# Kernel optimization log

Hardware: AMD Instinct MI355X
Metric: run time of the kernel (lower is better)

Reference implementation:

```python
import jax, jax.numpy as jnp
import numpy as np

# module constants (match init_kwargs)
D_MODEL = 1024
N_HEADS = 16
D_K = 64
CHUNK_LEN = 64
EPS = 1e-8

B, C, N, NL = 4, 16, 2, 128  # batch, chunks, neighbors, neighbor_len
S = C * CHUNK_LEN            # seq_len = 1024


def setup_inputs() -> dict:
    key = jax.random.key(0)
    ks = jax.random.split(key, 10)
    s = 0.02
    HD = N_HEADS * D_K
    return {
        "h": jax.random.normal(ks[0], (B, S, D_MODEL), jnp.float32),
        "e": jax.random.normal(ks[1], (B, C, N, NL, D_MODEL), jnp.float32),
        "g_norm": jnp.ones((D_MODEL,), jnp.float32),
        "Wq": jax.random.normal(ks[2], (D_MODEL, HD), jnp.float32) * s,
        "bq": jnp.zeros((HD,), jnp.float32),
        "Wk": jax.random.normal(ks[3], (D_MODEL, HD), jnp.float32) * s,
        "bk": jnp.zeros((HD,), jnp.float32),
        "Wv": jax.random.normal(ks[4], (D_MODEL, HD), jnp.float32) * s,
        "bv": jnp.zeros((HD,), jnp.float32),
        "Wo": jax.random.normal(ks[5], (HD, D_MODEL), jnp.float32) * s,
        "bo": jnp.zeros((D_MODEL,), jnp.float32),
    }


def _rmsnorm(x, g):
    return x * g * jax.lax.rsqrt(jnp.mean(x * x, axis=-1, keepdims=True) + EPS)


def reference(h, e, g_norm, Wq, bq, Wk, bk, Wv, bv, Wo, bo):
    b, seq, d = h.shape
    _, c, n, nl, _ = e.shape
    cl = CHUNK_LEN
    scale = 1.0 / np.sqrt(D_K).astype(np.float32)

    h_res = h
    hn = _rmsnorm(h[:, cl - 1:], g_norm)                 # [b, seq-cl+1, d]
    pad = c * cl - hn.shape[1]
    hn = jnp.pad(hn, ((0, 0), (0, pad), (0, 0)))         # [b, c*cl, d]
    hn = hn.reshape(b, c, cl, d)

    q = (hn @ Wq + bq).reshape(b, c, cl, N_HEADS, D_K)       # bcihd
    k = (e @ Wk + bk).reshape(b, c, n, nl, N_HEADS, D_K)     # bcnjhd
    v = (e @ Wv + bv).reshape(b, c, n, nl, N_HEADS, D_K)

    attn = jnp.einsum('bcihd,bcnjhd->bchinj', q, k) * scale  # [b,c,h,i,n,j]
    attn = jax.nn.softmax(attn.reshape(b, c, N_HEADS, cl, n * nl), axis=-1)
    attn = attn.reshape(b, c, N_HEADS, cl, n, nl)

    o = jnp.einsum('bchinj,bcnjhd->bcihd', attn, v)
    o = o.reshape(b, c * cl, N_HEADS * D_K)
    o = o @ Wo + bo                                          # [b, c*cl, d]
    o = jnp.pad(o, ((0, 0), (cl - 1, 0), (0, 0)))            # shift right by cl-1
    return o[:, :seq] + h_res
```

## Files before the change

kernel.cpp:

```cpp
#include <hip/hip_runtime.h>
#include <stdint.h>

#define DEV __device__ __forceinline__

typedef __attribute__((ext_vector_type(8))) __bf16 bf16x8;
typedef __attribute__((ext_vector_type(4))) float floatx4;

DEV float bf2f(unsigned short u) {
  union { unsigned int i; float f; } x; x.i = ((unsigned int)u) << 16; return x.f;
}
DEV unsigned int f2bf(float f) {
  union { float f; unsigned int i; } x; x.f = f;
  unsigned int r = x.i + 0x7FFFu + ((x.i >> 16) & 1u);
  return r >> 16;
}
DEV void gl2lds16(const unsigned short* g, unsigned short* l) {
  __builtin_amdgcn_global_load_lds(
      (const __attribute__((address_space(1))) unsigned int*)g,
      (__attribute__((address_space(3))) unsigned int*)l, 16, 0, 0);
}
DEV floatx4 zero4() { floatx4 z; z[0]=0.f; z[1]=0.f; z[2]=0.f; z[3]=0.f; return z; }

__global__ void cca_f2b_k(const float* __restrict__ x,
                          unsigned short* __restrict__ y) {
  int i = blockIdx.x * 256 + threadIdx.x;
  float4 v = ((const float4*)x)[i];
  uint2 o;
  o.x = f2bf(v.x) | (f2bf(v.y) << 16);
  o.y = f2bf(v.z) | (f2bf(v.w) << 16);
  ((uint2*)y)[i] = o;
}

__global__ void cca_transpose_k(const float* __restrict__ W,
                                unsigned short* __restrict__ Wt, int K, int N) {
  __shared__ float tile[64][65];
  int k0 = blockIdx.x * 64, n0 = blockIdx.y * 64;
  int t = threadIdx.x;
  int c = t & 63, r4 = t >> 6;
#pragma unroll
  for (int it = 0; it < 16; ++it) {
    int r = it * 4 + r4;
    tile[r][c] = W[(size_t)(k0 + r) * N + n0 + c];
  }
  __syncthreads();
#pragma unroll
  for (int it = 0; it < 16; ++it) {
    int r = it * 4 + r4;
    Wt[(size_t)(n0 + r) * K + k0 + c] = (unsigned short)f2bf(tile[c][r]);
  }
}

__global__ void cca_rmsnorm_k(const float* __restrict__ h,
                              const float* __restrict__ g,
                              unsigned short* __restrict__ hn) {
  int row = blockIdx.x;
  int b = row >> 10, p = row & 1023;
  int t = threadIdx.x;
  unsigned short* dst = hn + (size_t)row * 1024;
  if (p >= 961) {
    uint2 z; z.x = 0u; z.y = 0u;
    ((uint2*)dst)[t] = z;
    return;
  }
  const float* src = h + ((size_t)(b << 10) + p + 63) * 1024;
  float4 v = ((const float4*)src)[t];
  float ss = v.x*v.x + v.y*v.y + v.z*v.z + v.w*v.w;
#pragma unroll
  for (int m = 32; m > 0; m >>= 1) ss += __shfl_down(ss, m);
  __shared__ float wsum[4];
  int lane = t & 63, wv = t >> 6;
  if (lane == 0) wsum[wv] = ss;
  __syncthreads();
  float tot = wsum[0] + wsum[1] + wsum[2] + wsum[3];
  float r = rsqrtf(tot * (1.0f / 1024.0f) + 1e-8f);
  float4 gv = ((const float4*)g)[t];
  uint2 outp;
  outp.x = f2bf(v.x * gv.x * r) | (f2bf(v.y * gv.y * r) << 16);
  outp.y = f2bf(v.z * gv.z * r) | (f2bf(v.w * gv.w * r) << 16);
  ((uint2*)dst)[t] = outp;
}

template <int MODE>
__launch_bounds__(256, 2)
__global__ void cca_gemm_k(const unsigned short* __restrict__ A,
                           const unsigned short* __restrict__ Bt,
                           const float* __restrict__ bias1,
                           const float* __restrict__ bias2,
                           const float* __restrict__ resid,
                           void* __restrict__ Cout,
                           int M, int N, int K) {
  __shared__ unsigned short Ash[128 * 32];
  __shared__ unsigned short Bsh[128 * 32];
  int tM = blockIdx.x * 128, tN = blockIdx.y * 128;
  int t = threadIdx.x, lane = t & 63, wv = t >> 6;
  int wm = wv >> 1, wn = wv & 1;
  int l15 = lane & 15, quad = lane >> 4;
  int arow = lane >> 2, achk = lane & 3;
  floatx4 acc[4][4];
#pragma unroll
  for (int i = 0; i < 4; ++i)
#pragma unroll
    for (int j = 0; j < 4; ++j) acc[i][j] = zero4();

  for (int k0 = 0; k0 < K; k0 += 32) {
    __syncthreads();
#pragma unroll
    for (int ii = 0; ii < 2; ++ii) {
      int seg = wv + ii * 4;
      int row = seg * 16 + arow;
      gl2lds16(A + (size_t)(tM + row) * K + k0 + achk * 8, Ash + seg * 512);
      gl2lds16(Bt + (size_t)(tN + row) * K + k0 + achk * 8, Bsh + seg * 512);
    }
    __syncthreads();
    bf16x8 af[4], bfv[4];
#pragma unroll
    for (int mt = 0; mt < 4; ++mt)
      af[mt] = *(const bf16x8*)&Ash[(wm * 64 + mt * 16 + l15) * 32 + quad * 8];
#pragma unroll
    for (int nt = 0; nt < 4; ++nt)
      bfv[nt] = *(const bf16x8*)&Bsh[(wn * 64 + nt * 16 + l15) * 32 + quad * 8];
#pragma unroll
    for (int mt = 0; mt < 4; ++mt)
#pragma unroll
      for (int nt = 0; nt < 4; ++nt)
        acc[mt][nt] = __builtin_amdgcn_mfma_f32_16x16x32_bf16(af[mt], bfv[nt], acc[mt][nt], 0, 0, 0);
  }

#pragma unroll
  for (int mt = 0; mt < 4; ++mt) {
    int mrow = tM + wm * 64 + mt * 16 + quad * 4;
#pragma unroll
    for (int nt = 0; nt < 4; ++nt) {
      int ncol = tN + wn * 64 + nt * 16 + l15;
      float bs;
      if (MODE == 0) {
        bs = (bias2 != nullptr && ncol >= 1024) ? bias2[ncol - 1024] : bias1[ncol];
      } else {
        bs = bias1[ncol];
      }
#pragma unroll
      for (int r = 0; r < 4; ++r) {
        int m = mrow + r;
        float v = acc[mt][nt][r] + bs;
        if (MODE == 0) {
          ((unsigned short*)Cout)[(size_t)m * N + ncol] = (unsigned short)f2bf(v);
        } else {
          int p = m & 1023;
          if (p < 961) {
            size_t o = (size_t)(m + 63) * 1024 + (size_t)ncol;
            ((float*)Cout)[o] = v + resid[o];
          }
        }
      }
    }
  }
}

__launch_bounds__(256, 1)
__global__ void cca_attn_k(const unsigned short* __restrict__ Q,
                           const unsigned short* __restrict__ KV,
                           unsigned short* __restrict__ O) {
  __shared__ unsigned short Qsh[64 * 64];
  __shared__ unsigned short Ksh[256 * 64];
  __shared__ unsigned short VT[64 * 264];
  __shared__ unsigned short Psh[64 * 264];
  int bch = blockIdx.x;
  int hh = bch & 15, c = (bch >> 4) & 15, b = bch >> 8;
  int t = threadIdx.x, lane = t & 63, wv = t >> 6;
  int l15 = lane & 15, quad = lane >> 4;
  size_t qbase = (size_t)b * 1024 + (size_t)c * 64;
  size_t kvbase = (size_t)b * 4096 + (size_t)c * 256;
  int hoff = hh * 64;

  {
    int rowi = lane >> 3, chk = lane & 7;
#pragma unroll
    for (int ii = 0; ii < 2; ++ii) {
      int seg = wv + ii * 4;
      int row = seg * 8 + rowi;
      gl2lds16(Q + (qbase + row) * 1024 + hoff + chk * 8, Qsh + seg * 512);
    }
#pragma unroll
    for (int ii = 0; ii < 8; ++ii) {
      int seg = wv + ii * 4;
      int row = seg * 8 + rowi;
      gl2lds16(KV + (kvbase + row) * 2048 + hoff + chk * 8, Ksh + seg * 512);
    }
  }
  {
    const unsigned short* vp = KV + (kvbase + t) * 2048 + 1024 + hoff;
#pragma unroll
    for (int d0 = 0; d0 < 64; d0 += 8) {
      uint4 raw = *(const uint4*)(vp + d0);
      unsigned int w0 = raw.x, w1 = raw.y, w2 = raw.z, w3 = raw.w;
      VT[(d0 + 0) * 264 + t] = (unsigned short)(w0 & 0xffff);
      VT[(d0 + 1) * 264 + t] = (unsigned short)(w0 >> 16);
      VT[(d0 + 2) * 264 + t] = (unsigned short)(w1 & 0xffff);
      VT[(d0 + 3) * 264 + t] = (unsigned short)(w1 >> 16);
      VT[(d0 + 4) * 264 + t] = (unsigned short)(w2 & 0xffff);
      VT[(d0 + 5) * 264 + t] = (unsigned short)(w2 >> 16);
      VT[(d0 + 6) * 264 + t] = (unsigned short)(w3 & 0xffff);
      VT[(d0 + 7) * 264 + t] = (unsigned short)(w3 >> 16);
    }
  }
  __syncthreads();

  floatx4 st[16];
#pragma unroll
  for (int i = 0; i < 16; ++i) st[i] = zero4();
  bf16x8 a0 = *(const bf16x8*)&Qsh[(wv * 16 + l15) * 64 + quad * 8];
  bf16x8 a1 = *(const bf16x8*)&Qsh[(wv * 16 + l15) * 64 + 32 + quad * 8];
#pragma unroll
  for (int kt = 0; kt < 16; ++kt) {
    bf16x8 b0 = *(const bf16x8*)&Ksh[(kt * 16 + l15) * 64 + quad * 8];
    bf16x8 b1 = *(const bf16x8*)&Ksh[(kt * 16 + l15) * 64 + 32 + quad * 8];
    st[kt] = __builtin_amdgcn_mfma_f32_16x16x32_bf16(a0, b0, st[kt], 0, 0, 0);
    st[kt] = __builtin_amdgcn_mfma_f32_16x16x32_bf16(a1, b1, st[kt], 0, 0, 0);
  }

  const float scale = 0.125f;
#pragma unroll
  for (int r = 0; r < 4; ++r) {
    float mx = -1e30f;
#pragma unroll
    for (int kt = 0; kt < 16; ++kt) mx = fmaxf(mx, st[kt][r]);
    mx = fmaxf(mx, __shfl_xor(mx, 1));
    mx = fmaxf(mx, __shfl_xor(mx, 2));
    mx = fmaxf(mx, __shfl_xor(mx, 4));
    mx = fmaxf(mx, __shfl_xor(mx, 8));
    float sum = 0.f;
#pragma unroll
    for (int kt = 0; kt < 16; ++kt) {
      float e = __expf((st[kt][r] - mx) * scale);
      st[kt][r] = e;
      sum += e;
    }
    sum += __shfl_xor(sum, 1);
    sum += __shfl_xor(sum, 2);
    sum += __shfl_xor(sum, 4);
    sum += __shfl_xor(sum, 8);
    float inv = 1.0f / sum;
    int prow = wv * 16 + quad * 4 + r;
#pragma unroll
    for (int kt = 0; kt < 16; ++kt)
      Psh[prow * 264 + kt * 16 + l15] = (unsigned short)f2bf(st[kt][r] * inv);
  }

  floatx4 ot[4];
#pragma unroll
  for (int nt = 0; nt < 4; ++nt) ot[nt] = zero4();
#pragma unroll
  for (int kt2 = 0; kt2 < 8; ++kt2) {
    bf16x8 ap = *(const bf16x8*)&Psh[(wv * 16 + l15) * 264 + kt2 * 32 + quad * 8];
#pragma unroll
    for (int nt = 0; nt < 4; ++nt) {
      bf16x8 bv8 = *(const bf16x8*)&VT[(nt * 16 + l15) * 264 + kt2 * 32 + quad * 8];
      ot[nt] = __builtin_amdgcn_mfma_f32_16x16x32_bf16(ap, bv8, ot[nt], 0, 0, 0);
    }
  }
#pragma unroll
  for (int nt = 0; nt < 4; ++nt) {
#pragma unroll
    for (int r = 0; r < 4; ++r) {
      int i = wv * 16 + quad * 4 + r;
      int dcol = hoff + nt * 16 + l15;
      O[(qbase + i) * 1024 + dcol] = (unsigned short)f2bf(ot[nt][r]);
    }
  }
}

__global__ void cca_copyhead_k(const float* __restrict__ h,
                               float* __restrict__ out) {
  int idx = blockIdx.x * 256 + threadIdx.x;
  const int n4 = 4 * 63 * 1024 / 4;
  if (idx < n4) {
    int e4 = idx * 4;
    int b = e4 / (63 * 1024);
    int r = e4 - b * (63 * 1024);
    size_t off = (size_t)b * 1024 * 1024 + (size_t)r;
    *(float4*)(out + off) = *(const float4*)(h + off);
  }
}

extern "C" void kernel_launch(void* const* d_in, const int* in_sizes, int n_in,
                              void* d_out, int out_size, void* d_ws, size_t ws_size,
                              hipStream_t stream) {
  const float* h  = (const float*)d_in[0];
  const float* e  = (const float*)d_in[1];
  const float* g  = (const float*)d_in[2];
  const float* Wq = (const float*)d_in[3];
  const float* bq = (const float*)d_in[4];
  const float* Wk = (const float*)d_in[5];
  const float* bk = (const float*)d_in[6];
  const float* Wv = (const float*)d_in[7];
  const float* bv = (const float*)d_in[8];
  const float* Wo = (const float*)d_in[9];
  const float* bo = (const float*)d_in[10];
  float* out = (float*)d_out;

  unsigned short* ws   = (unsigned short*)d_ws;
  unsigned short* hn   = ws;
  unsigned short* WqT  = hn   + (size_t)4096 * 1024;
  unsigned short* WkvT = WqT  + (size_t)1024 * 1024;
  unsigned short* WoT  = WkvT + (size_t)2048 * 1024;
  unsigned short* Qb   = WoT  + (size_t)1024 * 1024;
  unsigned short* KVb  = Qb   + (size_t)4096 * 1024;
  unsigned short* Ob   = KVb  + (size_t)16384 * 2048;
  unsigned short* eb   = Ob   + (size_t)4096 * 1024;

  dim3 tgrid(16, 16);
  cca_transpose_k<<<tgrid, 256, 0, stream>>>(Wq, WqT, 1024, 1024);
  cca_transpose_k<<<tgrid, 256, 0, stream>>>(Wk, WkvT, 1024, 1024);
  cca_transpose_k<<<tgrid, 256, 0, stream>>>(Wv, WkvT + (size_t)1024 * 1024, 1024, 1024);
  cca_transpose_k<<<tgrid, 256, 0, stream>>>(Wo, WoT, 1024, 1024);

  cca_f2b_k<<<16384, 256, 0, stream>>>(e, eb);
  cca_rmsnorm_k<<<4096, 256, 0, stream>>>(h, g, hn);

  cca_gemm_k<0><<<dim3(32, 8), 256, 0, stream>>>(hn, WqT, bq, nullptr, nullptr,
                                                 (void*)Qb, 4096, 1024, 1024);
  cca_gemm_k<0><<<dim3(128, 16), 256, 0, stream>>>(eb, WkvT, bk, bv, nullptr,
                                                   (void*)KVb, 16384, 2048, 1024);

  cca_attn_k<<<1024, 256, 0, stream>>>(Qb, KVb, Ob);

  cca_gemm_k<1><<<dim3(32, 8), 256, 0, stream>>>(Ob, WoT, bo, nullptr, h,
                                                 (void*)out, 4096, 1024, 1024);
  cca_copyhead_k<<<252, 256, 0, stream>>>(h, out);
}
```

Before: 336.9 us.

## Merge prep kernels, swizzle GEMM LDS, and alias attention LDS for occupancy

The four weight transposes become one launch indexed by blockIdx.z. The bf16 conversion of e, the RMSNorm and the head copy become a single prep kernel, which cuts launch count and per-launch overhead. The GEMM now XOR-swizzles the 16-byte chunk index on both the global-to-LDS load and the fragment reads, to reduce LDS bank conflicts. Attention aliases Psh onto the Q/K buffer, with an added barrier, so LDS use drops enough to allow 2 blocks per CU under launch_bounds(256,2).

New measurement: 308.7 us. -8.4%, faster.

```diff
diff --git a/kernel.cpp b/kernel.cpp
--- a/kernel.cpp
+++ b/kernel.cpp
@@ -21,19 +21,23 @@
 }
 DEV floatx4 zero4() { floatx4 z; z[0]=0.f; z[1]=0.f; z[2]=0.f; z[3]=0.f; return z; }
 
-__global__ void cca_f2b_k(const float* __restrict__ x,
-                          unsigned short* __restrict__ y) {
-  int i = blockIdx.x * 256 + threadIdx.x;
-  float4 v = ((const float4*)x)[i];
-  uint2 o;
-  o.x = f2bf(v.x) | (f2bf(v.y) << 16);
-  o.y = f2bf(v.z) | (f2bf(v.w) << 16);
-  ((uint2*)y)[i] = o;
-}
-
-__global__ void cca_transpose_k(const float* __restrict__ W,
-                                unsigned short* __restrict__ Wt, int K, int N) {
+__global__ void cca_transpose_k(const float* __restrict__ W0,
+                                const float* __restrict__ W1,
+                                const float* __restrict__ W2,
+                                const float* __restrict__ W3,
+                                unsigned short* __restrict__ D0,
+                                unsigned short* __restrict__ D1,
+                                unsigned short* __restrict__ D2,
+                                unsigned short* __restrict__ D3) {
   __shared__ float tile[64][65];
+  const float* W; unsigned short* Wt;
+  switch (blockIdx.z) {
+    case 0: W = W0; Wt = D0; break;
+    case 1: W = W1; Wt = D1; break;
+    case 2: W = W2; Wt = D2; break;
+    default: W = W3; Wt = D3; break;
+  }
+  const int K = 1024, N = 1024;
   int k0 = blockIdx.x * 64, n0 = blockIdx.y * 64;
   int t = threadIdx.x;
   int c = t & 63, r4 = t >> 6;
@@ -50,34 +54,61 @@
   }
 }
 
-__global__ void cca_rmsnorm_k(const float* __restrict__ h,
-                              const float* __restrict__ g,
-                              unsigned short* __restrict__ hn) {
-  int row = blockIdx.x;
-  int b = row >> 10, p = row & 1023;
+__global__ void cca_prep_k(const float* __restrict__ e,
+                           unsigned short* __restrict__ eb,
+                           const float* __restrict__ h,
+                           const float* __restrict__ g,
+                           unsigned short* __restrict__ hn,
+                           float* __restrict__ out) {
+  int blk = blockIdx.x;
   int t = threadIdx.x;
-  unsigned short* dst = hn + (size_t)row * 1024;
-  if (p >= 961) {
-    uint2 z; z.x = 0u; z.y = 0u;
-    ((uint2*)dst)[t] = z;
+  if (blk < 16384) {
+    int i = blk * 256 + t;
+    float4 v = ((const float4*)e)[i];
+    uint2 o;
+    o.x = f2bf(v.x) | (f2bf(v.y) << 16);
+    o.y = f2bf(v.z) | (f2bf(v.w) << 16);
+    ((uint2*)eb)[i] = o;
     return;
   }
-  const float* src = h + ((size_t)(b << 10) + p + 63) * 1024;
-  float4 v = ((const float4*)src)[t];
-  float ss = v.x*v.x + v.y*v.y + v.z*v.z + v.w*v.w;
-#pragma unroll
-  for (int m = 32; m > 0; m >>= 1) ss += __shfl_down(ss, m);
-  __shared__ float wsum[4];
-  int lane = t & 63, wv = t >> 6;
-  if (lane == 0) wsum[wv] = ss;
-  __syncthreads();
-  float tot = wsum[0] + wsum[1] + wsum[2] + wsum[3];
-  float r = rsqrtf(tot * (1.0f / 1024.0f) + 1e-8f);
-  float4 gv = ((const float4*)g)[t];
-  uint2 outp;
-  outp.x = f2bf(v.x * gv.x * r) | (f2bf(v.y * gv.y * r) << 16);
-  outp.y = f2bf(v.z * gv.z * r) | (f2bf(v.w * gv.w * r) << 16);
-  ((uint2*)dst)[t] = outp;
+  if (blk < 20480) {
+    int row = blk - 16384;
+    int b = row >> 10, p = row & 1023;
+    unsigned short* dst = hn + (size_t)row * 1024;
+    if (p >= 961) {
+      uint2 z; z.x = 0u; z.y = 0u;
+      ((uint2*)dst)[t] = z;
+      return;
+    }
+    const float* src = h + ((size_t)(b << 10) + p + 63) * 1024;
+    float4 v = ((const float4*)src)[t];
+    float ss = v.x*v.x + v.y*v.y + v.z*v.z + v.w*v.w;
+#pragma unroll
+    for (int m = 32; m > 0; m >>= 1) ss += __shfl_down(ss, m);
+    __shared__ float wsum[4];
+    int lane = t & 63, wv = t >> 6;
+    if (lane == 0) wsum[wv] = ss;
+    __syncthreads();
+    float tot = wsum[0] + wsum[1] + wsum[2] + wsum[3];
+    float r = rsqrtf(tot * (1.0f / 1024.0f) + 1e-8f);
+    float4 gv = ((const float4*)g)[t];
+    uint2 outp;
+    outp.x = f2bf(v.x * gv.x * r) | (f2bf(v.y * gv.y * r) << 16);
+    outp.y = f2bf(v.z * gv.z * r) | (f2bf(v.w * gv.w * r) << 16);
+    ((uint2*)dst)[t] = outp;
+    return;
+  }
+  {
+    int idx = (blk - 20480) * 256 + t;
+    const int n4 = 4 * 63 * 1024 / 4;
+    if (idx < n4) {
+      int e4 = idx * 4;
+      int b = e4 / (63 * 1024);
+      int r = e4 - b * (63 * 1024);
+      size_t off = (size_t)b * 1024 * 1024 + (size_t)r;
+      *(float4*)(out + off) = *(const float4*)(h + off);
+    }
+  }
 }
 
 template <int MODE>
@@ -96,6 +127,8 @@
   int wm = wv >> 1, wn = wv & 1;
   int l15 = lane & 15, quad = lane >> 4;
   int arow = lane >> 2, achk = lane & 3;
+  int gchk = achk ^ ((arow >> 1) & 3);
+  int rchk = quad ^ ((l15 >> 1) & 3);
   floatx4 acc[4][4];
 #pragma unroll
   for (int i = 0; i < 4; ++i)
@@ -108,17 +141,17 @@
     for (int ii = 0; ii < 2; ++ii) {
       int seg = wv + ii * 4;
       int row = seg * 16 + arow;
-      gl2lds16(A + (size_t)(tM + row) * K + k0 + achk * 8, Ash + seg * 512);
-      gl2lds16(Bt + (size_t)(tN + row) * K + k0 + achk * 8, Bsh + seg * 512);
+      gl2lds16(A + (size_t)(tM + row) * K + k0 + gchk * 8, Ash + seg * 512);
+      gl2lds16(Bt + (size_t)(tN + row) * K + k0 + gchk * 8, Bsh + seg * 512);
     }
     __syncthreads();
     bf16x8 af[4], bfv[4];
 #pragma unroll
     for (int mt = 0; mt < 4; ++mt)
-      af[mt] = *(const bf16x8*)&Ash[(wm * 64 + mt * 16 + l15) * 32 + quad * 8];
+      af[mt] = *(const bf16x8*)&Ash[(wm * 64 + mt * 16 + l15) * 32 + rchk * 8];
 #pragma unroll
     for (int nt = 0; nt < 4; ++nt)
-      bfv[nt] = *(const bf16x8*)&Bsh[(wn * 64 + nt * 16 + l15) * 32 + quad * 8];
+      bfv[nt] = *(const bf16x8*)&Bsh[(wn * 64 + nt * 16 + l15) * 32 + rchk * 8];
 #pragma unroll
     for (int mt = 0; mt < 4; ++mt)
 #pragma unroll
@@ -156,14 +189,15 @@
   }
 }
 
-__launch_bounds__(256, 1)
+__launch_bounds__(256, 2)
 __global__ void cca_attn_k(const unsigned short* __restrict__ Q,
                            const unsigned short* __restrict__ KV,
                            unsigned short* __restrict__ O) {
-  __shared__ unsigned short Qsh[64 * 64];
-  __shared__ unsigned short Ksh[256 * 64];
+  __shared__ unsigned short smemA[64 * 64 + 256 * 64];
   __shared__ unsigned short VT[64 * 264];
-  __shared__ unsigned short Psh[64 * 264];
+  unsigned short* Qsh = smemA;
+  unsigned short* Ksh = smemA + 64 * 64;
+  unsigned short* Psh = smemA;
   int bch = blockIdx.x;
   int hh = bch & 15, c = (bch >> 4) & 15, b = bch >> 8;
   int t = threadIdx.x, lane = t & 63, wv = t >> 6;
@@ -217,6 +251,7 @@
     st[kt] = __builtin_amdgcn_mfma_f32_16x16x32_bf16(a0, b0, st[kt], 0, 0, 0);
     st[kt] = __builtin_amdgcn_mfma_f32_16x16x32_bf16(a1, b1, st[kt], 0, 0, 0);
   }
+  __syncthreads();
 
   const float scale = 0.125f;
 #pragma unroll
@@ -266,19 +301,6 @@
       int dcol = hoff + nt * 16 + l15;
       O[(qbase + i) * 1024 + dcol] = (unsigned short)f2bf(ot[nt][r]);
     }
-  }
-}
-
-__global__ void cca_copyhead_k(const float* __restrict__ h,
-                               float* __restrict__ out) {
-  int idx = blockIdx.x * 256 + threadIdx.x;
-  const int n4 = 4 * 63 * 1024 / 4;
-  if (idx < n4) {
-    int e4 = idx * 4;
-    int b = e4 / (63 * 1024);
-    int r = e4 - b * (63 * 1024);
-    size_t off = (size_t)b * 1024 * 1024 + (size_t)r;
-    *(float4*)(out + off) = *(const float4*)(h + off);
   }
 }
 
@@ -308,14 +330,10 @@
   unsigned short* Ob   = KVb  + (size_t)16384 * 2048;
   unsigned short* eb   = Ob   + (size_t)4096 * 1024;
 
-  dim3 tgrid(16, 16);
-  cca_transpose_k<<<tgrid, 256, 0, stream>>>(Wq, WqT, 1024, 1024);
-  cca_transpose_k<<<tgrid, 256, 0, stream>>>(Wk, WkvT, 1024, 1024);
-  cca_transpose_k<<<tgrid, 256, 0, stream>>>(Wv, WkvT + (size_t)1024 * 1024, 1024, 1024);
-  cca_transpose_k<<<tgrid, 256, 0, stream>>>(Wo, WoT, 1024, 1024);
-
-  cca_f2b_k<<<16384, 256, 0, stream>>>(e, eb);
-  cca_rmsnorm_k<<<4096, 256, 0, stream>>>(h, g, hn);
+  cca_transpose_k<<<dim3(16, 16, 4), 256, 0, stream>>>(
+      Wq, Wk, Wv, Wo, WqT, WkvT, WkvT + (size_t)1024 * 1024, WoT);
+
+  cca_prep_k<<<20732, 256, 0, stream>>>(e, eb, h, g, hn, out);
 
   cca_gemm_k<0><<<dim3(32, 8), 256, 0, stream>>>(hn, WqT, bq, nullptr, nullptr,
                                                  (void*)Qb, 4096, 1024, 1024);
@@ -326,5 +344,4 @@
 
   cca_gemm_k<1><<<dim3(32, 8), 256, 0, stream>>>(Ob, WoT, bo, nullptr, h,
                                                  (void*)out, 4096, 1024, 1024);
-  cca_copyhead_k<<<252, 256, 0, stream>>>(h, out);
-}
+}
```
